# Performance work log

Measured on AMD Instinct MI355X. Metric: run time of the kernel, lower is better.

## Reference

```python
import jax, jax.numpy as jnp
import numpy as np

K = 9
PAD = K // 2


def _conv1d(x, w):
    # x: (B, C, L), w: (Cout, Cin, K) -> (B, Cout, L), 'same' padding, no bias
    return jax.lax.conv_general_dilated(
        x, w, window_strides=(1,), padding=((PAD, PAD),),
        dimension_numbers=('NCH', 'OIH', 'NCH'))


def _propagate(x, w, axis, reverse):
    # Sequential message passing along `axis` of (B, C, H, W):
    #   out[0] = x[0]; out[i] = x[i] + relu(conv1d(out[i-1]))
    xm = jnp.moveaxis(x, axis, 0)  # (L, B, C, other)
    if reverse:
        xm = xm[::-1]

    def step(prev, cur):
        new = cur + jax.nn.relu(_conv1d(prev, w))
        return new, new

    _, outs = jax.lax.scan(step, xm[0], xm[1:])
    res = jnp.concatenate([xm[:1], outs], axis=0)
    if reverse:
        res = res[::-1]
    return jnp.moveaxis(res, 0, axis)


def setup_inputs() -> dict:
    key = jax.random.key(0)
    ks = jax.random.split(key, 5)
    B, C, H, W = 16, 128, 72, 200
    scale = 1.0 / np.sqrt(C * K)  # kaiming-ish fan-in init
    x = jax.random.normal(ks[0], (B, C, H, W), dtype=jnp.float32)
    w_down = jax.random.normal(ks[1], (C, C, K), dtype=jnp.float32) * scale
    w_up = jax.random.normal(ks[2], (C, C, K), dtype=jnp.float32) * scale
    w_right = jax.random.normal(ks[3], (C, C, K), dtype=jnp.float32) * scale
    w_left = jax.random.normal(ks[4], (C, C, K), dtype=jnp.float32) * scale
    return {'x': x, 'w_down': w_down, 'w_up': w_up,
            'w_right': w_right, 'w_left': w_left}


def reference(x, w_down, w_up, w_right, w_left):
    # down: top->bottom over H; up: bottom->top over H;
    # right: left->right over W; left: right->left over W.
    x = _propagate(x, w_down, 2, False)
    x = _propagate(x, w_up, 2, True)
    x = _propagate(x, w_right, 3, False)
    x = _propagate(x, w_left, 3, True)
    return x
```

## Files before the change

### kernel.cpp

```cpp
#include <hip/hip_runtime.h>
#include <cstdint>
#include <cstddef>


#define B_ 16
#define C_ 128
#define H_ 72
#define W_ 200
#define KW 9
#define NTOT (B_ * C_ * H_ * W_)

using f16x8 = _Float16 __attribute__((ext_vector_type(8)));
using f32x4 = float __attribute__((ext_vector_type(4)));

#define N_AGPR_FRAGS 28

__device__ __forceinline__ unsigned pack_h2(_Float16 lo, _Float16 hi) {
  unsigned short a = __builtin_bit_cast(unsigned short, lo);
  unsigned short b = __builtin_bit_cast(unsigned short, hi);
  return (unsigned)a | ((unsigned)b << 16);
}

__device__ __forceinline__ float dev_load(const float* p) {
  return __hip_atomic_load(p, __ATOMIC_RELAXED, __HIP_MEMORY_SCOPE_AGENT);
}
__device__ __forceinline__ void dev_store(float* p, float v) {
  __hip_atomic_store(p, v, __ATOMIC_RELAXED, __HIP_MEMORY_SCOPE_AGENT);
}

__global__ void copy_f4(const float4* __restrict__ src, float4* __restrict__ dst, int n4) {
  int i = blockIdx.x * blockDim.x + threadIdx.x;
  const int stride = gridDim.x * blockDim.x;
  for (; i < n4; i += stride) dst[i] = src[i];
}

template <int SH, int SW>
__global__ void transpose_hw(const float* __restrict__ src, float* __restrict__ dst) {
  __shared__ float t[32][33];
  const size_t base = (size_t)blockIdx.z * SH * SW;
  const int x = blockIdx.x * 32 + threadIdx.x;
#pragma unroll
  for (int j = 0; j < 4; ++j) {
    const int y = blockIdx.y * 32 + threadIdx.y + j * 8;
    if (y < SH && x < SW) t[threadIdx.y + j * 8][threadIdx.x] = src[base + (size_t)y * SW + x];
  }
  __syncthreads();
  const int x2 = blockIdx.y * 32 + threadIdx.x;
#pragma unroll
  for (int j = 0; j < 4; ++j) {
    const int y2 = blockIdx.x * 32 + threadIdx.y + j * 8;
    if (y2 < SW && x2 < SH) dst[base + (size_t)y2 * SH + x2] = t[threadIdx.x][threadIdx.y + j * 8];
  }
}

__global__ void repack_w(const float* __restrict__ wgt, f16x8* __restrict__ whi,
                         f16x8* __restrict__ wlo) {
  const int blk = blockIdx.x;
  const int cot = blk / 36, t = blk % 36;
  const int lane = threadIdx.x;
  const int n = lane & 15, q = lane >> 4;
  const int co = cot * 16 + n, dk = t >> 2, ci0 = (t & 3) * 32 + q * 8;
  f16x8 h, l;
#pragma unroll
  for (int j = 0; j < 8; ++j) {
    const float w = wgt[((size_t)co * C_ + ci0 + j) * KW + dk];
    const _Float16 hh = (_Float16)w;
    h[j] = hh;
    l[j] = (_Float16)(w - (float)hh);
  }
  whi[(size_t)blk * 64 + lane] = h;
  wlo[(size_t)blk * 64 + lane] = l;
}

template <int RDIM, int WDIM, int NCH>
__global__ __launch_bounds__(512, 1) void pass_mfma(float* __restrict__ data,
                                                    const f16x8* __restrict__ whi,
                                                    const f16x8* __restrict__ wlo,
                                                    unsigned* flags, const int dir) {
  constexpr int RW = RDIM * WDIM;
  constexpr int PL = 24 * 68;
  __shared__ __align__(16) unsigned fh[2 * PL];
  __shared__ __align__(16) unsigned fl[2 * PL];

  const int tid = threadIdx.x;
  const int wave = tid >> 6, lane = tid & 63;
  const int n = lane & 15, q = lane >> 4;
  const int b = blockIdx.x & 15, jc = blockIdx.x >> 4;
  const int pos_base = jc * 16;
  const int pos = pos_base + n;
  const size_t bbase = (size_t)b * C_ * RW;

  f16x8 ahi[36];
#pragma unroll
  for (int t = 0; t < 36; ++t) ahi[t] = whi[(size_t)(wave * 36 + t) * 64 + lane];
  const f16x8* wloL = wlo + (size_t)wave * 36 * 64 + lane;

  const int h_wi8 = tid >> 6, h_c2 = tid & 63;
  const int h_wi = (h_wi8 < 4) ? h_wi8 : (h_wi8 + 16);
  const int h_p = pos_base - 4 + h_wi;
  const bool h_valid = (h_p >= 0 && h_p < WDIM);
  const int h_jn = (h_wi < 4) ? (jc - 1) : (jc + 1);

  {
    const int r0 = (dir > 0) ? 0 : (RDIM - 1);
#pragma unroll
    for (int i = 0; i < 3; ++i) {
      const int idx = tid + 512 * i;
      const int wi = idx >> 6, c2 = idx & 63;
      const int p = pos_base - 4 + wi;
      float x0 = 0.f, x1 = 0.f;
      if (p >= 0 && p < WDIM) {
        x0 = data[bbase + (size_t)(2 * c2) * RW + (size_t)r0 * WDIM + p];
        x1 = data[bbase + (size_t)(2 * c2 + 1) * RW + (size_t)r0 * WDIM + p];
      }
      const _Float16 h0 = (_Float16)x0, h1 = (_Float16)x1;
      const _Float16 l0 = (_Float16)(x0 - (float)h0), l1 = (_Float16)(x1 - (float)h1);
      fh[wi * 68 + c2] = pack_h2(h0, h1);
      fl[wi * 68 + c2] = pack_h2(l0, l1);
    }
  }
  __syncthreads();

  for (int s = 1; s < RDIM; ++s) {
    const int r = (dir > 0) ? s : (RDIM - 1 - s);
    const int rp = r - dir;
    const int pb = (s - 1) & 1;
    const int cb = s & 1;

#pragma unroll
    for (int t = 0; t < N_AGPR_FRAGS; ++t) asm volatile("" : "+a"(ahi[t]));

    float cur[4];
#pragma unroll
    for (int reg = 0; reg < 4; ++reg) {
      const int co = wave * 16 + q * 4 + reg;
      cur[reg] = (pos < WDIM) ? data[bbase + (size_t)co * RW + (size_t)r * WDIM + pos] : 0.f;
    }

    if (s > 1) {
      float x0 = 0.f, x1 = 0.f;
      if (h_valid) {
        unsigned* f = &flags[((size_t)b * RDIM + rp) * NCH + h_jn];
        while (__hip_atomic_load(f, __ATOMIC_RELAXED, __HIP_MEMORY_SCOPE_AGENT) == 0u)
          __builtin_amdgcn_s_sleep(1);
        x0 = dev_load(&data[bbase + (size_t)(2 * h_c2) * RW + (size_t)rp * WDIM + h_p]);
        x1 = dev_load(&data[bbase + (size_t)(2 * h_c2 + 1) * RW + (size_t)rp * WDIM + h_p]);
      }
      const _Float16 h0 = (_Float16)x0, h1 = (_Float16)x1;
      const _Float16 l0 = (_Float16)(x0 - (float)h0), l1 = (_Float16)(x1 - (float)h1);
      fh[pb * PL + h_wi * 68 + h_c2] = pack_h2(h0, h1);
      fl[pb * PL + h_wi * 68 + h_c2] = pack_h2(l0, l1);
    }
    __syncthreads();

    f32x4 aA = {0.f, 0.f, 0.f, 0.f}, aB = {0.f, 0.f, 0.f, 0.f}, aC = {0.f, 0.f, 0.f, 0.f};
#pragma unroll
    for (int t = 0; t < 36; ++t) {
      const int dk = t >> 2;
      const int off = pb * PL + (n + dk) * 68 + (t & 3) * 16 + q * 4;
      const f16x8 bh = *(const f16x8*)&fh[off];
      const f16x8 bl = *(const f16x8*)&fl[off];
      const f16x8 al = wloL[(size_t)t * 64];
      aA = __builtin_amdgcn_mfma_f32_16x16x32_f16(ahi[t], bh, aA, 0, 0, 0);
      aB = __builtin_amdgcn_mfma_f32_16x16x32_f16(ahi[t], bl, aB, 0, 0, 0);
      aC = __builtin_amdgcn_mfma_f32_16x16x32_f16(al, bh, aC, 0, 0, 0);
    }

    float resv[4];
#pragma unroll
    for (int reg = 0; reg < 4; ++reg) {
      const float v = aA[reg] + aB[reg] + aC[reg];
      resv[reg] = (pos < WDIM) ? (cur[reg] + fmaxf(v, 0.f)) : 0.f;
    }
    if (pos < WDIM) {
#pragma unroll
      for (int reg = 0; reg < 4; ++reg) {
        const int co = wave * 16 + q * 4 + reg;
        dev_store(&data[bbase + (size_t)co * RW + (size_t)r * WDIM + pos], resv[reg]);
      }
    }
    {
      const int base = cb * PL + (n + 4) * 68 + wave * 8 + q * 2;
      const _Float16 h0 = (_Float16)resv[0], h1 = (_Float16)resv[1];
      const _Float16 l0 = (_Float16)(resv[0] - (float)h0), l1 = (_Float16)(resv[1] - (float)h1);
      fh[base] = pack_h2(h0, h1);
      fl[base] = pack_h2(l0, l1);
      const _Float16 h2 = (_Float16)resv[2], h3 = (_Float16)resv[3];
      const _Float16 l2 = (_Float16)(resv[2] - (float)h2), l3 = (_Float16)(resv[3] - (float)h3);
      fh[base + 1] = pack_h2(h2, h3);
      fl[base + 1] = pack_h2(l2, l3);
    }
    __syncthreads();
    if (tid == 0)
      __hip_atomic_store(&flags[((size_t)b * RDIM + r) * NCH + jc], 1u, __ATOMIC_RELAXED,
                         __HIP_MEMORY_SCOPE_AGENT);
  }
}

extern "C" void kernel_launch(void* const* d_in, const int* in_sizes, int n_in, void* d_out,
                              int out_size, void* d_ws, size_t ws_size, hipStream_t stream) {
  const float* x = (const float*)d_in[0];
  const float* w_down = (const float*)d_in[1];
  const float* w_up = (const float*)d_in[2];
  const float* w_right = (const float*)d_in[3];
  const float* w_left = (const float*)d_in[4];
  float* out = (float*)d_out;

  unsigned* flags = (unsigned*)d_ws;
  unsigned* f_down = flags;
  unsigned* f_up = f_down + H_ * 13 * B_;
  unsigned* f_right = f_up + H_ * 13 * B_;
  unsigned* f_left = f_right + W_ * 5 * B_;
  hipMemsetAsync(d_ws, 0, 262144, stream);

  const size_t PLANE = (size_t)8 * 36 * 64;
  f16x8* wf = (f16x8*)((char*)d_ws + 262144);
  f16x8* whi_d = wf + 0 * PLANE;
  f16x8* wlo_d = wf + 1 * PLANE;
  f16x8* whi_u = wf + 2 * PLANE;
  f16x8* wlo_u = wf + 3 * PLANE;
  f16x8* whi_r = wf + 4 * PLANE;
  f16x8* wlo_r = wf + 5 * PLANE;
  f16x8* whi_l = wf + 6 * PLANE;
  f16x8* wlo_l = wf + 7 * PLANE;

  const size_t toff = 262144 + 8 * PLANE * sizeof(f16x8);
  const size_t tbytes = (size_t)NTOT * sizeof(float);
  float* T = (ws_size >= toff + tbytes) ? (float*)((char*)d_ws + toff) : (float*)d_in[0];

  repack_w<<<288, 64, 0, stream>>>(w_down, whi_d, wlo_d);
  repack_w<<<288, 64, 0, stream>>>(w_up, whi_u, wlo_u);
  repack_w<<<288, 64, 0, stream>>>(w_right, whi_r, wlo_r);
  repack_w<<<288, 64, 0, stream>>>(w_left, whi_l, wlo_l);

  copy_f4<<<1024, 256, 0, stream>>>((const float4*)x, (float4*)out, NTOT / 4);

  pass_mfma<H_, W_, 13><<<16 * 13, 512, 0, stream>>>(out, whi_d, wlo_d, f_down, +1);
  pass_mfma<H_, W_, 13><<<16 * 13, 512, 0, stream>>>(out, whi_u, wlo_u, f_up, -1);

  {
    dim3 g((W_ + 31) / 32, (H_ + 31) / 32, B_ * C_);
    transpose_hw<H_, W_><<<g, dim3(32, 8), 0, stream>>>(out, T);
  }

  pass_mfma<W_, H_, 5><<<16 * 5, 512, 0, stream>>>(T, whi_r, wlo_r, f_right, +1);
  pass_mfma<W_, H_, 5><<<16 * 5, 512, 0, stream>>>(T, whi_l, wlo_l, f_left, -1);

  {
    dim3 g((H_ + 31) / 32, (W_ + 31) / 32, B_ * C_);
    transpose_hw<W_, H_><<<g, dim3(32, 8), 0, stream>>>(T, out);
  }
}
```

Before: 3.637 ms.

## Exchange halo columns via compact packed-fp16 staging ring buffer

Each block now writes its edge columns, already split into packed fp16 hi/lo pairs, into a small per-batch staging ring buffer in the workspace. Neighbouring blocks read that buffer instead of gathering strided fp32 values from the main tensor, so they no longer redo the hi/lo split. Main data stores become plain stores instead of device-scope atomics. The 4-deep ring keyed by step parity relies on the flag protocol to keep neighbours from running more than a few steps apart. It also moves the T buffer offset in the workspace.

```diff
diff --git a/kernel.cpp b/kernel.cpp
--- a/kernel.cpp
+++ b/kernel.cpp
@@ -14,6 +14,8 @@
 using f32x4 = float __attribute__((ext_vector_type(4)));
 
 #define N_AGPR_FRAGS 28
+#define NCH_MAX 13
+#define STG_PER_B (4 * NCH_MAX * 2 * 512)
 
 __device__ __forceinline__ unsigned pack_h2(_Float16 lo, _Float16 hi) {
   unsigned short a = __builtin_bit_cast(unsigned short, lo);
@@ -21,10 +23,10 @@
   return (unsigned)a | ((unsigned)b << 16);
 }
 
-__device__ __forceinline__ float dev_load(const float* p) {
+__device__ __forceinline__ unsigned dev_load_u32(const unsigned* p) {
   return __hip_atomic_load(p, __ATOMIC_RELAXED, __HIP_MEMORY_SCOPE_AGENT);
 }
-__device__ __forceinline__ void dev_store(float* p, float v) {
+__device__ __forceinline__ void dev_store_u32(unsigned* p, unsigned v) {
   __hip_atomic_store(p, v, __ATOMIC_RELAXED, __HIP_MEMORY_SCOPE_AGENT);
 }
 
@@ -76,7 +78,8 @@
 __global__ __launch_bounds__(512, 1) void pass_mfma(float* __restrict__ data,
                                                     const f16x8* __restrict__ whi,
                                                     const f16x8* __restrict__ wlo,
-                                                    unsigned* flags, const int dir) {
+                                                    unsigned* flags, unsigned* stg,
+                                                    const int dir) {
   constexpr int RW = RDIM * WDIM;
   constexpr int PL = 24 * 68;
   __shared__ __align__(16) unsigned fh[2 * PL];
@@ -89,6 +92,7 @@
   const int pos_base = jc * 16;
   const int pos = pos_base + n;
   const size_t bbase = (size_t)b * C_ * RW;
+  unsigned* stgB = stg + (size_t)b * STG_PER_B;
 
   f16x8 ahi[36];
 #pragma unroll
@@ -100,6 +104,8 @@
   const int h_p = pos_base - 4 + h_wi;
   const bool h_valid = (h_p >= 0 && h_p < WDIM);
   const int h_jn = (h_wi < 4) ? (jc - 1) : (jc + 1);
+  const int h_side = (h_wi8 < 4) ? 1 : 0;
+  const int h_wip = (h_wi8 < 4) ? h_wi8 : (h_wi8 - 4);
 
   {
     const int r0 = (dir > 0) ? 0 : (RDIM - 1);
@@ -138,18 +144,18 @@
     }
 
     if (s > 1) {
-      float x0 = 0.f, x1 = 0.f;
+      unsigned uh = 0, ul = 0;
       if (h_valid) {
         unsigned* f = &flags[((size_t)b * RDIM + rp) * NCH + h_jn];
         while (__hip_atomic_load(f, __ATOMIC_RELAXED, __HIP_MEMORY_SCOPE_AGENT) == 0u)
           __builtin_amdgcn_s_sleep(1);
-        x0 = dev_load(&data[bbase + (size_t)(2 * h_c2) * RW + (size_t)rp * WDIM + h_p]);
-        x1 = dev_load(&data[bbase + (size_t)(2 * h_c2 + 1) * RW + (size_t)rp * WDIM + h_p]);
-      }
-      const _Float16 h0 = (_Float16)x0, h1 = (_Float16)x1;
-      const _Float16 l0 = (_Float16)(x0 - (float)h0), l1 = (_Float16)(x1 - (float)h1);
-      fh[pb * PL + h_wi * 68 + h_c2] = pack_h2(h0, h1);
-      fl[pb * PL + h_wi * 68 + h_c2] = pack_h2(l0, l1);
+        const unsigned* sb = stgB +
+            ((size_t)(((s - 1) & 3) * NCH + h_jn) * 2 + h_side) * 512 + h_wip * 64 + h_c2;
+        uh = dev_load_u32(sb);
+        ul = dev_load_u32(sb + 256);
+      }
+      fh[pb * PL + h_wi * 68 + h_c2] = uh;
+      fl[pb * PL + h_wi * 68 + h_c2] = ul;
     }
     __syncthreads();
 
@@ -176,19 +182,31 @@
 #pragma unroll
       for (int reg = 0; reg < 4; ++reg) {
         const int co = wave * 16 + q * 4 + reg;
-        dev_store(&data[bbase + (size_t)co * RW + (size_t)r * WDIM + pos], resv[reg]);
+        data[bbase + (size_t)co * RW + (size_t)r * WDIM + pos] = resv[reg];
       }
     }
     {
-      const int base = cb * PL + (n + 4) * 68 + wave * 8 + q * 2;
       const _Float16 h0 = (_Float16)resv[0], h1 = (_Float16)resv[1];
       const _Float16 l0 = (_Float16)(resv[0] - (float)h0), l1 = (_Float16)(resv[1] - (float)h1);
-      fh[base] = pack_h2(h0, h1);
-      fl[base] = pack_h2(l0, l1);
       const _Float16 h2 = (_Float16)resv[2], h3 = (_Float16)resv[3];
       const _Float16 l2 = (_Float16)(resv[2] - (float)h2), l3 = (_Float16)(resv[3] - (float)h3);
-      fh[base + 1] = pack_h2(h2, h3);
-      fl[base + 1] = pack_h2(l2, l3);
+      const unsigned uh0 = pack_h2(h0, h1), uh1 = pack_h2(h2, h3);
+      const unsigned ul0 = pack_h2(l0, l1), ul1 = pack_h2(l2, l3);
+      const int base = cb * PL + (n + 4) * 68 + wave * 8 + q * 2;
+      fh[base] = uh0;
+      fh[base + 1] = uh1;
+      fl[base] = ul0;
+      fl[base + 1] = ul1;
+      if (n < 4 || n >= 12) {
+        const int side = (n < 4) ? 0 : 1;
+        const int wip = (n < 4) ? n : (n - 12);
+        unsigned* sb = stgB + ((size_t)((s & 3) * NCH + jc) * 2 + side) * 512 + wip * 64 +
+                       (wave * 8 + q * 2);
+        dev_store_u32(sb, uh0);
+        dev_store_u32(sb + 1, uh1);
+        dev_store_u32(sb + 256, ul0);
+        dev_store_u32(sb + 256 + 1, ul1);
+      }
     }
     __syncthreads();
     if (tid == 0)
@@ -224,7 +242,9 @@
   f16x8* whi_l = wf + 6 * PLANE;
   f16x8* wlo_l = wf + 7 * PLANE;
 
-  const size_t toff = 262144 + 8 * PLANE * sizeof(f16x8);
+  unsigned* stg = (unsigned*)((char*)d_ws + 2621440);
+
+  const size_t toff = 2621440 + (size_t)B_ * STG_PER_B * 4;
   const size_t tbytes = (size_t)NTOT * sizeof(float);
   float* T = (ws_size >= toff + tbytes) ? (float*)((char*)d_ws + toff) : (float*)d_in[0];
 
@@ -235,16 +255,16 @@
 
   copy_f4<<<1024, 256, 0, stream>>>((const float4*)x, (float4*)out, NTOT / 4);
 
-  pass_mfma<H_, W_, 13><<<16 * 13, 512, 0, stream>>>(out, whi_d, wlo_d, f_down, +1);
-  pass_mfma<H_, W_, 13><<<16 * 13, 512, 0, stream>>>(out, whi_u, wlo_u, f_up, -1);
+  pass_mfma<H_, W_, 13><<<16 * 13, 512, 0, stream>>>(out, whi_d, wlo_d, f_down, stg, +1);
+  pass_mfma<H_, W_, 13><<<16 * 13, 512, 0, stream>>>(out, whi_u, wlo_u, f_up, stg, -1);
 
   {
     dim3 g((W_ + 31) / 32, (H_ + 31) / 32, B_ * C_);
     transpose_hw<H_, W_><<<g, dim3(32, 8), 0, stream>>>(out, T);
   }
 
-  pass_mfma<W_, H_, 5><<<16 * 5, 512, 0, stream>>>(T, whi_r, wlo_r, f_right, +1);
-  pass_mfma<W_, H_, 5><<<16 * 5, 512, 0, stream>>>(T, whi_l, wlo_l, f_left, -1);
+  pass_mfma<W_, H_, 5><<<16 * 5, 512, 0, stream>>>(T, whi_r, wlo_r, f_right, stg, +1);
+  pass_mfma<W_, H_, 5><<<16 * 5, 512, 0, stream>>>(T, whi_l, wlo_l, f_left, stg, -1);
 
   {
     dim3 g((H_ + 31) / 32, (W_ + 31) / 32, B_ * C_);
```

Result: no change. 3.656 ms (+0.5%).
